# Optimization experiments

Measured on AMD Instinct MI355X. Metric: run time of the kernel, lower is better.

Reference implementation:

```python
import jax, jax.numpy as jnp
import numpy as np

B, C, H, W = 32, 3, 512, 512
EPS = 1e-8


def _radius_bins(h, w):
    cy, cx = h // 2, w // 2
    y = jnp.arange(h, dtype=jnp.float32) - cy
    x = jnp.arange(w, dtype=jnp.float32) - cx
    radius = jnp.sqrt(y[:, None] ** 2 + x[None, :] ** 2)  # [H, W]
    max_r = min(cy, cx)
    bins = jnp.floor(radius).astype(jnp.int32)
    # pixels with radius >= max_r fall outside all bins in the original loop;
    # route them to a dummy overflow bin that we drop afterwards.
    bins = jnp.where(bins < max_r, bins, max_r)
    return bins.reshape(-1), max_r


def _psd(x):
    f = jnp.fft.fft2(x)                  # over last two dims, like torch.fft.fft2
    psd = jnp.abs(f) ** 2
    return jnp.log(psd + EPS)            # log_power=True


def _radial_average(psd):
    b, c, h, w = psd.shape
    bins, max_r = _radius_bins(h, w)     # [H*W], static
    data = psd.reshape(b * c, h * w).T   # [H*W, B*C]
    sums = jax.ops.segment_sum(data, bins, num_segments=max_r + 1)
    counts = jax.ops.segment_sum(jnp.ones((h * w,), psd.dtype), bins,
                                 num_segments=max_r + 1)
    avg = jnp.where(counts[:, None] > 0, sums / counts[:, None], 0.0)
    avg = avg[:max_r]                    # drop overflow bin -> [max_r, B*C]
    return avg.T.reshape(b, c, max_r)


def setup_inputs() -> dict:
    key = jax.random.key(0)
    k1, k2 = jax.random.split(key)
    predicted = jax.random.normal(k1, (B, C, H, W), dtype=jnp.float32)
    target = jax.random.normal(k2, (B, C, H, W), dtype=jnp.float32)
    return {"predicted": predicted, "target": target}


def reference(predicted, target):
    pred_rad = _radial_average(_psd(predicted))
    targ_rad = _radial_average(_psd(target))
    return jnp.mean(jnp.abs(pred_rad - targ_rad))  # l1, reduction='mean'
```

## Files before the change

kernel.cpp:

```cpp
#include <hip/hip_runtime.h>
#include <math.h>

#define HH 512
#define WW 512
#define IMG (HH*WW)
#define NIMG_PER 96
#define NIMG 192
#define NBIN 256
#define EPSV 1e-8f
#define LN2F 0.69314718055994530942f

#define CSTR 264
#define IMGC (512*CSTR)
#define NT16 17
#define SLOT 575

typedef float v2f  __attribute__((ext_vector_type(2)));
typedef _Float16 h2f __attribute__((ext_vector_type(2)));

__device__ __forceinline__ int drev(int s) {
    return ((s & 7) << 6) | (s & 56) | (s >> 6);
}
__device__ __forceinline__ int fsw(int a) { return a + (a >> 3); }

__device__ __forceinline__ v2f cmul(v2f a, v2f b) {
    return (v2f){a.x, a.x} * b + (v2f){a.y, a.y} * (v2f){-b.y, b.x};
}
__device__ __forceinline__ v2f cni(v2f a) { return (v2f){a.y, -a.x}; }

__device__ __forceinline__ v2f h2tof(unsigned int u) {
    h2f h = __builtin_bit_cast(h2f, u);
    return (v2f){(float)h.x, (float)h.y};
}
__device__ __forceinline__ unsigned int ftoh2(v2f v) {
    return __builtin_bit_cast(unsigned int, __builtin_amdgcn_cvt_pkrtz(v.x, v.y));
}

__device__ __forceinline__ void wsync() {
    asm volatile("" ::: "memory");
    __builtin_amdgcn_wave_barrier();
    asm volatile("" ::: "memory");
}

__device__ __forceinline__ void bfly8(v2f x[8]) {
    const float R = 0.70710678118654752440f;
    v2f t0=x[0]+x[4], t4=x[0]-x[4];
    v2f t1=x[1]+x[5], t5=x[1]-x[5];
    v2f t2=x[2]+x[6], t6=x[2]-x[6];
    v2f t3=x[3]+x[7], t7=x[3]-x[7];
    v2f u0=t0+t2, u2=t0-t2;
    v2f u1=t1+t3, u3=t1-t3;
    x[0]=u0+u1; x[4]=u0-u1;
    { v2f n3 = cni(u3); x[2]=u2+n3; x[6]=u2-n3; }
    v2f s1 = (v2f){R, R} * ((v2f){t5.x, t5.y} + (v2f){t5.y, -t5.x});
    v2f s2 = cni(t6);
    v2f s3 = (v2f){R, R} * ((v2f){t7.y, -t7.x} - (v2f){t7.x, t7.y});
    v2f v0=t4+s2, v2_=t4-s2;
    v2f v1=s1+s3, v3=s1-s3;
    x[1]=v0+v1; x[5]=v0-v1;
    { v2f m3 = cni(v3); x[3]=v2_+m3; x[7]=v2_-m3; }
}

__device__ __forceinline__ void twiddle7(v2f* x, float ang) {
    const float sn = __sinf(ang), cs = __cosf(ang);
    const v2f w1 = (v2f){cs, sn};
    const v2f w2 = cmul(w1, w1);
    const v2f w3 = cmul(w2, w1);
    const v2f w4 = cmul(w2, w2);
    const v2f w5 = cmul(w2, w3);
    const v2f w6 = cmul(w3, w3);
    const v2f w7 = cmul(w3, w4);
    x[1]=cmul(x[1],w1); x[2]=cmul(x[2],w2); x[3]=cmul(x[3],w3);
    x[4]=cmul(x[4],w4); x[5]=cmul(x[5],w5); x[6]=cmul(x[6],w6);
    x[7]=cmul(x[7],w7);
}

__global__ __launch_bounds__(512) void rowfft_kernel(
    const float* __restrict__ pred, const float* __restrict__ targ,
    unsigned int* __restrict__ out, int img_base)
{
    __shared__ v2f sd[8*SLOT];
    const int t    = threadIdx.x;
    const int lane = t & 63;
    const int w    = t >> 6;

    const int pb = blockIdx.x;
    const int li = blockIdx.y;
    const int g  = img_base + li;
    const float* img = (g < NIMG_PER) ? (pred + (size_t)g * IMG)
                                      : (targ + (size_t)(g - NIMG_PER) * IMG);
    const float* rowA = img + (size_t)(pb*16 + 2*w) * WW + lane;
    const float* rowB = rowA + WW;

    v2f* p = sd + w * SLOT;
    v2f x[8];
    const int i = lane;

    #pragma unroll
    for (int j = 0; j < 8; ++j)
        x[j] = (v2f){rowA[64*j], rowB[64*j]};
    bfly8(x);
    twiddle7(x, -0.012271846303085130f * (float)i);
    {
        v2f* q = p + fsw(i);
        #pragma unroll
        for (int j = 0; j < 8; ++j) q[72*j] = x[j];
    }
    wsync();

    {
        v2f* q = p + 72*(i >> 3) + (i & 7);
        #pragma unroll
        for (int j = 0; j < 8; ++j) x[j] = q[9*j];
        bfly8(x);
        twiddle7(x, -0.098174770424681038f * (float)(i & 7));
        #pragma unroll
        for (int j = 0; j < 8; ++j) q[9*j] = x[j];
    }
    wsync();

    {
        v2f* q = p + 9*i;
        #pragma unroll
        for (int j = 0; j < 8; ++j) x[j] = q[j];
        bfly8(x);
        #pragma unroll
        for (int j = 0; j < 8; ++j) q[j] = x[j];
    }
    wsync();

    unsigned int* dstA = out + (size_t)g * IMGC + (size_t)(pb*16 + 2*w) * CSTR;
    unsigned int* dstB = dstA + CSTR;
    #pragma unroll
    for (int it = 0; it < 5; ++it) {
        const int k = it*64 + lane;
        if (k <= 256) {
            const v2f P = p[fsw(drev(k))];
            const v2f Q = p[fsw(drev((512 - k) & 511))];
            const v2f Fa = (v2f){0.5f, 0.5f} * (P + (v2f){Q.x, -Q.y});
            const v2f Fb = (v2f){0.5f, 0.5f} * ((v2f){P.y, -P.x} + (v2f){Q.y, Q.x});
            dstA[k] = ftoh2(Fa);
            dstB[k] = ftoh2(Fb);
        } else if (k < CSTR) {
            dstA[k] = 0u;
            dstB[k] = 0u;
        }
    }
}

__global__ __launch_bounds__(512) void colfft_kernel(
    const unsigned int* __restrict__ in, float* __restrict__ bins2, int img_base)
{
    __shared__ uint2 sd[8*SLOT];
    __shared__ float bs[4*257];
    const int t    = threadIdx.x;
    const int lane = t & 63;
    const int w    = t >> 6;

    for (int id = t; id < 4*257; id += 512) bs[id] = 0.0f;

    const int li = blockIdx.y;
    const int x0 = blockIdx.x * 16;
    {
        const int y0 = t >> 2;
        const int c  = t & 3;
        int cb = x0 + 4*c;
        if (cb > CSTR - 4) cb = CSTR - 4;
        const uint4* gsrc = (const uint4*)(in + (size_t)li * IMGC
                                              + (size_t)y0 * CSTR + cb);
        uint2* d0 = sd + (2*c + 0)*SLOT + fsw(y0);
        uint2* d1 = d0 + SLOT;
        #pragma unroll
        for (int it = 0; it < 4; ++it) {
            const uint4 v = gsrc[(size_t)it * 128 * (CSTR/4)];
            d0[144*it] = make_uint2(v.x, v.y);
            d1[144*it] = make_uint2(v.z, v.w);
        }
    }
    __syncthreads();

    uint2* p = sd + w * SLOT;
    v2f a[8], b[8];
    const int i = lane;

    {
        uint2* q = p + fsw(i);
        #pragma unroll
        for (int j = 0; j < 8; ++j) {
            const uint2 u = q[72*j];
            a[j] = h2tof(u.x); b[j] = h2tof(u.y);
        }
        bfly8(a); bfly8(b);
        const float ang = -0.012271846303085130f * (float)i;
        const float sn = __sinf(ang), cs = __cosf(ang);
        const v2f w1 = (v2f){cs, sn};
        const v2f w2 = cmul(w1,w1), w3 = cmul(w2,w1), w4 = cmul(w2,w2);
        const v2f w5 = cmul(w2,w3), w6 = cmul(w3,w3), w7 = cmul(w3,w4);
        a[1]=cmul(a[1],w1); b[1]=cmul(b[1],w1);
        a[2]=cmul(a[2],w2); b[2]=cmul(b[2],w2);
        a[3]=cmul(a[3],w3); b[3]=cmul(b[3],w3);
        a[4]=cmul(a[4],w4); b[4]=cmul(b[4],w4);
        a[5]=cmul(a[5],w5); b[5]=cmul(b[5],w5);
        a[6]=cmul(a[6],w6); b[6]=cmul(b[6],w6);
        a[7]=cmul(a[7],w7); b[7]=cmul(b[7],w7);
        #pragma unroll
        for (int j = 0; j < 8; ++j) q[72*j] = make_uint2(ftoh2(a[j]), ftoh2(b[j]));
    }
    wsync();

    {
        uint2* q = p + 72*(i >> 3) + (i & 7);
        #pragma unroll
        for (int j = 0; j < 8; ++j) {
            const uint2 u = q[9*j];
            a[j] = h2tof(u.x); b[j] = h2tof(u.y);
        }
        bfly8(a); bfly8(b);
        const float ang = -0.098174770424681038f * (float)(i & 7);
        const float sn = __sinf(ang), cs = __cosf(ang);
        const v2f w1 = (v2f){cs, sn};
        const v2f w2 = cmul(w1,w1), w3 = cmul(w2,w1), w4 = cmul(w2,w2);
        const v2f w5 = cmul(w2,w3), w6 = cmul(w3,w3), w7 = cmul(w3,w4);
        a[1]=cmul(a[1],w1); b[1]=cmul(b[1],w1);
        a[2]=cmul(a[2],w2); b[2]=cmul(b[2],w2);
        a[3]=cmul(a[3],w3); b[3]=cmul(b[3],w3);
        a[4]=cmul(a[4],w4); b[4]=cmul(b[4],w4);
        a[5]=cmul(a[5],w5); b[5]=cmul(b[5],w5);
        a[6]=cmul(a[6],w6); b[6]=cmul(b[6],w6);
        a[7]=cmul(a[7],w7); b[7]=cmul(b[7],w7);
        #pragma unroll
        for (int j = 0; j < 8; ++j) q[9*j] = make_uint2(ftoh2(a[j]), ftoh2(b[j]));
    }
    wsync();

    {
        uint2* q = p + 9*i;
        #pragma unroll
        for (int j = 0; j < 8; ++j) {
            const uint2 u = q[j];
            a[j] = h2tof(u.x); b[j] = h2tof(u.y);
        }
        bfly8(a); bfly8(b);
        #pragma unroll
        for (int j = 0; j < 8; ++j) q[j] = make_uint2(ftoh2(a[j]), ftoh2(b[j]));
    }
    wsync();

    {
        const int h   = lane;
        const int kxA = x0 + 2*w;
        const int kxB = kxA + 1;
        const bool vA = (kxA <= 256), vB = (kxB <= 256);
        const float sA = (kxA == 0 || kxA == 256) ? 0.5f : 1.0f;
        const float sB = (kxB == 256) ? 0.5f : 1.0f;
        const float dxA = (float)((kxA - 256) * (kxA - 256));
        const float dxB = (float)((kxB - 256) * (kxB - 256));
        float* bsw = bs + (w & 3) * 257;
        uint2* q = p + fsw(8*(h & 7) + (h >> 3));
        float dyf = (float)(8*h - 256);

        float accA = 0.0f, accB = 0.0f;
        int pbA = 1000, pbB = 1000;
        #pragma unroll
        for (int j = 0; j < 8; ++j) {
            const uint2 u = q[72*j];
            const v2f va = h2tof(u.x);
            const v2f vb = h2tof(u.y);
            const float la = __log2f(fmaf(va.x, va.x, fmaf(va.y, va.y, EPSV)));
            const float lb = __log2f(fmaf(vb.x, vb.x, fmaf(vb.y, vb.y, EPSV)));
            const int bA = (int)sqrtf(fmaf(dyf, dyf, dxA));
            const int bB = (int)sqrtf(fmaf(dyf, dyf, dxB));
            dyf += 1.0f;
            if (bA != pbA) {
                if (pbA < NBIN && vA) atomicAdd(&bsw[pbA], accA * sA);
                pbA = bA; accA = la;
            } else accA += la;
            if (bB != pbB) {
                if (pbB < NBIN && vB) atomicAdd(&bsw[pbB], accB * sB);
                pbB = bB; accB = lb;
            } else accB += lb;
        }
        if (pbA < NBIN && vA) atomicAdd(&bsw[pbA], accA * sA);
        if (pbB < NBIN && vB) atomicAdd(&bsw[pbB], accB * sB);
    }
    __syncthreads();

    if (t < NBIN) {
        float v = 0.0f;
        #pragma unroll
        for (int r = 0; r < 4; ++r) v += bs[r*257 + t];
        bins2[((size_t)blockIdx.x * NIMG + (img_base + li)) * NBIN + t] = 2.0f * v;
    }
}

__global__ __launch_bounds__(256) void reduce_kernel(
    const float* __restrict__ bins2, float* __restrict__ bins)
{
    const int li = blockIdx.x;
    const int t  = threadIdx.x;
    float s = 0.0f;
    #pragma unroll
    for (int tile = 0; tile < NT16; ++tile)
        s += bins2[((size_t)tile * NIMG + li) * NBIN + t];
    bins[(size_t)li * NBIN + t] = s;
}

__global__ __launch_bounds__(256) void counts_kernel(float* __restrict__ cnt)
{
    __shared__ float c[NBIN];
    const int t = threadIdx.x;
    c[t] = 0.0f;
    __syncthreads();

    const int base = blockIdx.x * 4096;
    #pragma unroll
    for (int i = 0; i < 16; ++i) {
        const int id = base + i * 256 + t;
        const int y = id >> 9, xx = id & 511;
        const int dy = y - 256, dx = xx - 256;
        const int b  = (int)sqrtf((float)(dy*dy + dx*dx));
        if (b < NBIN) atomicAdd(&c[b], 1.0f);
    }
    __syncthreads();
    if (c[t] != 0.0f) atomicAdd(&cnt[t], c[t]);
}

__global__ __launch_bounds__(256) void finalize_kernel(
    const float* __restrict__ bins, const float* __restrict__ cnt,
    float* __restrict__ out)
{
    __shared__ float red[256];
    const int t = threadIdx.x;

    float acc = 0.0f;
    for (int id = t; id < NIMG_PER * NBIN; id += 256) {
        const int i = id >> 8;
        const int r = id & 255;
        const float d = fabsf(bins[(size_t)i * NBIN + r]
                            - bins[(size_t)(NIMG_PER + i) * NBIN + r]);
        acc += d / cnt[r];
    }
    red[t] = acc;
    __syncthreads();
    for (int w = 128; w > 0; w >>= 1) {
        if (t < w) red[t] += red[t + w];
        __syncthreads();
    }
    if (t == 0) out[0] = red[0] * (LN2F / (float)(NIMG_PER * NBIN));
}

extern "C" void kernel_launch(void* const* d_in, const int* in_sizes, int n_in,
                              void* d_out, int out_size, void* d_ws, size_t ws_size,
                              hipStream_t stream)
{
    const float* pred = (const float*)d_in[0];
    const float* targ = (const float*)d_in[1];
    float* out = (float*)d_out;

    char* ws = (char*)d_ws;
    float* cnt   = (float*)ws;
    float* bins  = cnt + NBIN;
    float* bins2 = bins + (size_t)NIMG * NBIN;
    const size_t fixed_f = NBIN + (size_t)NIMG*NBIN + (size_t)NT16*NIMG*NBIN;
    const size_t off = (fixed_f*sizeof(float) + 255) & ~(size_t)255;
    unsigned int* cbuf = (unsigned int*)(ws + off);

    const size_t per_img = (size_t)IMGC * sizeof(unsigned int);
    size_t avail = (ws_size > off) ? (ws_size - off) : 0;
    int chunk = (int)(avail / per_img);
    if (chunk > NIMG) chunk = NIMG;
    if (chunk < 1) chunk = 1;

    hipMemsetAsync(cnt, 0, NBIN * sizeof(float), stream);
    counts_kernel<<<dim3(64), dim3(256), 0, stream>>>(cnt);

    for (int base = 0; base < NIMG; base += chunk) {
        const int n = (NIMG - base < chunk) ? (NIMG - base) : chunk;
        dim3 gA(HH / 16, n), gB(NT16, n);
        rowfft_kernel<<<gA, dim3(512), 0, stream>>>(pred, targ, cbuf, base);
        colfft_kernel<<<gB, dim3(512), 0, stream>>>(cbuf, bins2, base);
    }

    reduce_kernel<<<dim3(NIMG), dim3(256), 0, stream>>>(bins2, bins);
    finalize_kernel<<<dim3(1), dim3(256), 0, stream>>>(bins, cnt, out);
}
```

Before: 211.3 us.

## Load column FFT inputs directly to registers and bin from registers

The column FFT kernel now has each wavefront read its column pair straight from global memory into registers. This removes the cooperative staging into shared memory and the block-wide barrier. The final radix stage keeps results in registers and bins them directly, dropping a shared-memory write/read round trip and the run-length accumulation logic. Each wave gets its own histogram slice, which uses more LDS and issues one atomic per element, and the strided per-column global loads may coalesce worse than the old uint4 loads.

```diff
diff --git a/kernel.cpp b/kernel.cpp
--- a/kernel.cpp
+++ b/kernel.cpp
@@ -75,6 +75,20 @@
     x[7]=cmul(x[7],w7);
 }
 
+__device__ __forceinline__ void twiddle7x2(v2f* a, v2f* b, float ang) {
+    const float sn = __sinf(ang), cs = __cosf(ang);
+    const v2f w1 = (v2f){cs, sn};
+    const v2f w2 = cmul(w1,w1), w3 = cmul(w2,w1), w4 = cmul(w2,w2);
+    const v2f w5 = cmul(w2,w3), w6 = cmul(w3,w3), w7 = cmul(w3,w4);
+    a[1]=cmul(a[1],w1); b[1]=cmul(b[1],w1);
+    a[2]=cmul(a[2],w2); b[2]=cmul(b[2],w2);
+    a[3]=cmul(a[3],w3); b[3]=cmul(b[3],w3);
+    a[4]=cmul(a[4],w4); b[4]=cmul(b[4],w4);
+    a[5]=cmul(a[5],w5); b[5]=cmul(b[5],w5);
+    a[6]=cmul(a[6],w6); b[6]=cmul(b[6],w6);
+    a[7]=cmul(a[7],w7); b[7]=cmul(b[7],w7);
+}
+
 __global__ __launch_bounds__(512) void rowfft_kernel(
     const float* __restrict__ pred, const float* __restrict__ targ,
     unsigned int* __restrict__ out, int img_base)
@@ -152,57 +166,34 @@
     const unsigned int* __restrict__ in, float* __restrict__ bins2, int img_base)
 {
     __shared__ uint2 sd[8*SLOT];
-    __shared__ float bs[4*257];
+    __shared__ float bs[8*257];
     const int t    = threadIdx.x;
     const int lane = t & 63;
     const int w    = t >> 6;
-
-    for (int id = t; id < 4*257; id += 512) bs[id] = 0.0f;
-
-    const int li = blockIdx.y;
-    const int x0 = blockIdx.x * 16;
-    {
-        const int y0 = t >> 2;
-        const int c  = t & 3;
-        int cb = x0 + 4*c;
-        if (cb > CSTR - 4) cb = CSTR - 4;
-        const uint4* gsrc = (const uint4*)(in + (size_t)li * IMGC
-                                              + (size_t)y0 * CSTR + cb);
-        uint2* d0 = sd + (2*c + 0)*SLOT + fsw(y0);
-        uint2* d1 = d0 + SLOT;
-        #pragma unroll
-        for (int it = 0; it < 4; ++it) {
-            const uint4 v = gsrc[(size_t)it * 128 * (CSTR/4)];
-            d0[144*it] = make_uint2(v.x, v.y);
-            d1[144*it] = make_uint2(v.z, v.w);
-        }
-    }
-    __syncthreads();
-
+    const int i    = lane;
+
+    for (int id = lane; id < 257; id += 64) bs[w*257 + id] = 0.0f;
+
+    const int li  = blockIdx.y;
+    const int x0  = blockIdx.x * 16;
+    const int kxA = x0 + 2*w;
+    const int kxL = (kxA > 262) ? 262 : kxA;
+
+    v2f a[8], b[8];
+
+    {
+        const uint2* colp = (const uint2*)(in + (size_t)li * IMGC) + (kxL >> 1);
+        #pragma unroll
+        for (int j = 0; j < 8; ++j) {
+            const uint2 u = colp[(size_t)(i + 64*j) * (CSTR/2)];
+            a[j] = h2tof(u.x); b[j] = h2tof(u.y);
+        }
+    }
+    bfly8(a); bfly8(b);
+    twiddle7x2(a, b, -0.012271846303085130f * (float)i);
     uint2* p = sd + w * SLOT;
-    v2f a[8], b[8];
-    const int i = lane;
-
     {
         uint2* q = p + fsw(i);
-        #pragma unroll
-        for (int j = 0; j < 8; ++j) {
-            const uint2 u = q[72*j];
-            a[j] = h2tof(u.x); b[j] = h2tof(u.y);
-        }
-        bfly8(a); bfly8(b);
-        const float ang = -0.012271846303085130f * (float)i;
-        const float sn = __sinf(ang), cs = __cosf(ang);
-        const v2f w1 = (v2f){cs, sn};
-        const v2f w2 = cmul(w1,w1), w3 = cmul(w2,w1), w4 = cmul(w2,w2);
-        const v2f w5 = cmul(w2,w3), w6 = cmul(w3,w3), w7 = cmul(w3,w4);
-        a[1]=cmul(a[1],w1); b[1]=cmul(b[1],w1);
-        a[2]=cmul(a[2],w2); b[2]=cmul(b[2],w2);
-        a[3]=cmul(a[3],w3); b[3]=cmul(b[3],w3);
-        a[4]=cmul(a[4],w4); b[4]=cmul(b[4],w4);
-        a[5]=cmul(a[5],w5); b[5]=cmul(b[5],w5);
-        a[6]=cmul(a[6],w6); b[6]=cmul(b[6],w6);
-        a[7]=cmul(a[7],w7); b[7]=cmul(b[7],w7);
         #pragma unroll
         for (int j = 0; j < 8; ++j) q[72*j] = make_uint2(ftoh2(a[j]), ftoh2(b[j]));
     }
@@ -216,18 +207,7 @@
             a[j] = h2tof(u.x); b[j] = h2tof(u.y);
         }
         bfly8(a); bfly8(b);
-        const float ang = -0.098174770424681038f * (float)(i & 7);
-        const float sn = __sinf(ang), cs = __cosf(ang);
-        const v2f w1 = (v2f){cs, sn};
-        const v2f w2 = cmul(w1,w1), w3 = cmul(w2,w1), w4 = cmul(w2,w2);
-        const v2f w5 = cmul(w2,w3), w6 = cmul(w3,w3), w7 = cmul(w3,w4);
-        a[1]=cmul(a[1],w1); b[1]=cmul(b[1],w1);
-        a[2]=cmul(a[2],w2); b[2]=cmul(b[2],w2);
-        a[3]=cmul(a[3],w3); b[3]=cmul(b[3],w3);
-        a[4]=cmul(a[4],w4); b[4]=cmul(b[4],w4);
-        a[5]=cmul(a[5],w5); b[5]=cmul(b[5],w5);
-        a[6]=cmul(a[6],w6); b[6]=cmul(b[6],w6);
-        a[7]=cmul(a[7],w7); b[7]=cmul(b[7],w7);
+        twiddle7x2(a, b, -0.098174770424681038f * (float)(i & 7));
         #pragma unroll
         for (int j = 0; j < 8; ++j) q[9*j] = make_uint2(ftoh2(a[j]), ftoh2(b[j]));
     }
@@ -241,54 +221,33 @@
             a[j] = h2tof(u.x); b[j] = h2tof(u.y);
         }
         bfly8(a); bfly8(b);
-        #pragma unroll
-        for (int j = 0; j < 8; ++j) q[j] = make_uint2(ftoh2(a[j]), ftoh2(b[j]));
-    }
-    wsync();
-
-    {
-        const int h   = lane;
-        const int kxA = x0 + 2*w;
+
         const int kxB = kxA + 1;
         const bool vA = (kxA <= 256), vB = (kxB <= 256);
         const float sA = (kxA == 0 || kxA == 256) ? 0.5f : 1.0f;
         const float sB = (kxB == 256) ? 0.5f : 1.0f;
         const float dxA = (float)((kxA - 256) * (kxA - 256));
         const float dxB = (float)((kxB - 256) * (kxB - 256));
-        float* bsw = bs + (w & 3) * 257;
-        uint2* q = p + fsw(8*(h & 7) + (h >> 3));
-        float dyf = (float)(8*h - 256);
-
-        float accA = 0.0f, accB = 0.0f;
-        int pbA = 1000, pbB = 1000;
+        float* bsw = bs + w*257;
+        const int kyb = 8*(i & 7) + (i >> 3);
+
         #pragma unroll
         for (int j = 0; j < 8; ++j) {
-            const uint2 u = q[72*j];
-            const v2f va = h2tof(u.x);
-            const v2f vb = h2tof(u.y);
-            const float la = __log2f(fmaf(va.x, va.x, fmaf(va.y, va.y, EPSV)));
-            const float lb = __log2f(fmaf(vb.x, vb.x, fmaf(vb.y, vb.y, EPSV)));
+            const float dyf = (float)(64*j + kyb - 256);
+            const float la = __log2f(fmaf(a[j].x, a[j].x, fmaf(a[j].y, a[j].y, EPSV)));
+            const float lb = __log2f(fmaf(b[j].x, b[j].x, fmaf(b[j].y, b[j].y, EPSV)));
             const int bA = (int)sqrtf(fmaf(dyf, dyf, dxA));
             const int bB = (int)sqrtf(fmaf(dyf, dyf, dxB));
-            dyf += 1.0f;
-            if (bA != pbA) {
-                if (pbA < NBIN && vA) atomicAdd(&bsw[pbA], accA * sA);
-                pbA = bA; accA = la;
-            } else accA += la;
-            if (bB != pbB) {
-                if (pbB < NBIN && vB) atomicAdd(&bsw[pbB], accB * sB);
-                pbB = bB; accB = lb;
-            } else accB += lb;
-        }
-        if (pbA < NBIN && vA) atomicAdd(&bsw[pbA], accA * sA);
-        if (pbB < NBIN && vB) atomicAdd(&bsw[pbB], accB * sB);
+            if (vA && bA < NBIN) atomicAdd(&bsw[bA], la * sA);
+            if (vB && bB < NBIN) atomicAdd(&bsw[bB], lb * sB);
+        }
     }
     __syncthreads();
 
     if (t < NBIN) {
         float v = 0.0f;
         #pragma unroll
-        for (int r = 0; r < 4; ++r) v += bs[r*257 + t];
+        for (int r = 0; r < 8; ++r) v += bs[r*257 + t];
         bins2[((size_t)blockIdx.x * NIMG + (img_base + li)) * NBIN + t] = 2.0f * v;
     }
 }
```

Result: slower. 232.2 us (+9.9%).
